# Kernel optimization log

Measured on AMD Instinct MI355X. Metric: run time of the kernel, lower is better.

## Reference

```python
import jax, jax.numpy as jnp
import numpy as np
import math

NUM_HEADS = 16
D_MODEL = 1024
LN_EPS = 1e-5


def _layer_norm(x, g, b):
    mu = jnp.mean(x, axis=-1, keepdims=True)
    var = jnp.mean((x - mu) ** 2, axis=-1, keepdims=True)
    return (x - mu) / jnp.sqrt(var + LN_EPS) * g + b


def setup_inputs() -> dict:
    key = jax.random.key(0)
    ks = jax.random.split(key, 12)
    B, H, W, d = 32, 16, 16, D_MODEL
    P, F = 64, 128
    s = 0.02
    return {
        "x": jax.random.normal(ks[0], (B, H, W, d), jnp.float32),
        "pattern_features": jax.random.normal(ks[1], (B, P, F), jnp.float32),
        "wq": jax.random.normal(ks[2], (d, d), jnp.float32) * s,
        "bq": jnp.zeros((d,), jnp.float32),
        "wk": jax.random.normal(ks[3], (d, d), jnp.float32) * s,
        "bk": jnp.zeros((d,), jnp.float32),
        "wv": jax.random.normal(ks[4], (d, d), jnp.float32) * s,
        "bv": jnp.zeros((d,), jnp.float32),
        "wo": jax.random.normal(ks[5], (d, d), jnp.float32) * s,
        "bo": jnp.zeros((d,), jnp.float32),
        "ln_g": jnp.ones((d,), jnp.float32),
        "ln_b": jnp.zeros((d,), jnp.float32),
    }


def reference(x, pattern_features, wq, bq, wk, bk, wv, bv, wo, bo, ln_g, ln_b):
    B, H, W, d = x.shape
    S = H * W
    nh = NUM_HEADS
    dk = d // nh
    x_seq = x.reshape(B, S, d)

    def proj(w, b):
        return (x_seq @ w.T + b).reshape(B, S, nh, dk).transpose(0, 2, 1, 3)  # (B,nh,S,dk)

    q, k, v = proj(wq, bq), proj(wk, bk), proj(wv, bv)
    scores = jnp.einsum("bhsd,bhtd->bhst", q, k) / math.sqrt(dk)  # (B,nh,S,S)

    # creative bias: diversity bonus on top-left min(S,64) block, same for all heads
    m = min(S, 64)
    sim = jnp.einsum("bpf,bqf->bpq", pattern_features, pattern_features)
    div = 1.0 - jax.nn.softmax(sim, axis=-1)  # (B,P,P)
    bias = jnp.zeros((B, nh, S, S), x.dtype)
    bias = bias.at[:, :, :m, :m].set(div[:, None, :m, :m] * 0.1)

    # faithful to torch: scores + bias.unsqueeze(0) -> rank-5 (1,B,nh,S,S)
    scores5 = scores[None] + bias[None]
    aw = jax.nn.softmax(scores5, axis=-1)
    attn = jnp.matmul(aw, v)  # (1,B,nh,S,dk) via broadcasting
    # faithful to torch transpose(1,2).view(B,S,d): row-major reshape of (1,nh,B,S,dk)
    attn = jnp.transpose(attn, (0, 2, 1, 3, 4)).reshape(B, S, d)

    out = attn @ wo.T + bo
    out = _layer_norm(out + x_seq, ln_g, ln_b)

    attention_weights = jax.nn.softmax(scores, axis=-1).mean(axis=1)  # (B,S,S)
    return out.reshape(B, H, W, d), attention_weights
```

## Files before the change

kernel.cpp:

```cpp
#include <hip/hip_runtime.h>

typedef unsigned short u16;
typedef unsigned int   u32;
typedef short bf16x8 __attribute__((ext_vector_type(8)));
typedef float f32x4  __attribute__((ext_vector_type(4)));

__device__ __forceinline__ float bf2f(u16 u){
  union { u32 u; float f; } c; c.u = ((u32)u) << 16; return c.f;
}
__device__ __forceinline__ u16 f2bf(float f){
  union { float f; u32 u; } c; c.f = f;
  u32 u = c.u + 0x7fffu + ((c.u >> 16) & 1u);
  return (u16)(u >> 16);
}

__device__ __forceinline__ void gload16(const u16* g, u16* l){
  __builtin_amdgcn_global_load_lds((const __attribute__((address_space(1))) u32*)g,
                                   (__attribute__((address_space(3))) u32*)l, 16, 0, 0);
}

__device__ __forceinline__ float waveRed(float v, int ismax){
  #pragma unroll
  for (int o = 32; o > 0; o >>= 1){
    float t = __shfl_xor(v, o, 64);
    v = ismax ? fmaxf(v, t) : (v + t);
  }
  return v;
}
__device__ __forceinline__ float blockRed(float v, int ismax, float* red, int tid){
  v = waveRed(v, ismax);
  __syncthreads();
  if ((tid & 63) == 0) red[tid >> 6] = v;
  __syncthreads();
  return ismax ? fmaxf(fmaxf(red[0], red[1]), fmaxf(red[2], red[3]))
               : (red[0] + red[1] + red[2] + red[3]);
}

__global__ __launch_bounds__(256)
void conv_x(const float* __restrict__ src, u16* __restrict__ dst){
  const size_t i = ((size_t)blockIdx.x * 256 + threadIdx.x) * 8;
  const float4 a = *(const float4*)(src + i);
  const float4 b = *(const float4*)(src + i + 4);
  uint4 o;
  o.x = (u32)f2bf(a.x) | ((u32)f2bf(a.y) << 16);
  o.y = (u32)f2bf(a.z) | ((u32)f2bf(a.w) << 16);
  o.z = (u32)f2bf(b.x) | ((u32)f2bf(b.y) << 16);
  o.w = (u32)f2bf(b.z) | ((u32)f2bf(b.w) << 16);
  *(uint4*)(dst + i) = o;
}

__global__ __launch_bounds__(256)
void conv_w4(const float* __restrict__ w0, const float* __restrict__ w1,
             const float* __restrict__ w2, const float* __restrict__ w3,
             u16* __restrict__ dst){
  const float* s = blockIdx.y == 0 ? w0 : (blockIdx.y == 1 ? w1 : (blockIdx.y == 2 ? w2 : w3));
  u16* d = dst + (size_t)blockIdx.y * 1048576;
  const size_t i = ((size_t)blockIdx.x * 256 + threadIdx.x) * 8;
  const float4 a = *(const float4*)(s + i);
  const float4 b = *(const float4*)(s + i + 4);
  uint4 o;
  o.x = (u32)f2bf(a.x) | ((u32)f2bf(a.y) << 16);
  o.y = (u32)f2bf(a.z) | ((u32)f2bf(a.w) << 16);
  o.z = (u32)f2bf(b.x) | ((u32)f2bf(b.y) << 16);
  o.w = (u32)f2bf(b.z) | ((u32)f2bf(b.w) << 16);
  *(uint4*)(d + i) = o;
}

__global__ __launch_bounds__(256)
void div_kernel(const float* __restrict__ pf, float* __restrict__ divp)
{
  __shared__ float pfs[64][129];
  __shared__ float svs[64][65];
  const int b = blockIdx.x;
  const int tid = threadIdx.x;
  const float* pb = pf + (size_t)b * 8192;
  for (int i = tid; i < 8192; i += 256) pfs[i >> 7][i & 127] = pb[i];
  __syncthreads();
  const int p = tid & 63, qg = tid >> 6;
  for (int qq = qg * 16; qq < qg * 16 + 16; ++qq){
    float a = 0.f;
    #pragma unroll 8
    for (int f = 0; f < 128; ++f) a += pfs[p][f] * pfs[qq][f];
    svs[p][qq] = a;
  }
  __syncthreads();
  if (tid < 64){
    float m = -1e30f;
    for (int qq = 0; qq < 64; ++qq) m = fmaxf(m, svs[tid][qq]);
    float s = 0.f;
    for (int qq = 0; qq < 64; ++qq){ const float e = __expf(svs[tid][qq] - m); svs[tid][qq] = e; s += e; }
    const float inv = 1.f / s;
    float* dr = divp + ((size_t)b * 64 + tid) * 64;
    for (int qq = 0; qq < 64; ++qq) dr[qq] = 0.1f * (1.f - svs[tid][qq] * inv);
  }
}

template<int MODE>
__global__ __launch_bounds__(256, 3)
void gemm_lds(const u16* __restrict__ A, const u16* __restrict__ Wb,
              const float* __restrict__ bias0, const float* __restrict__ bias1,
              const float* __restrict__ bias2, void* __restrict__ outp)
{
  __shared__ u16 As[3][4096];
  __shared__ u16 Bs[3][4096];
  const int tid = threadIdx.x, lane = tid & 63, w = tid >> 6;
  const int wm = (w >> 1) * 64, wn = (w & 1) * 64;
  const int bm = blockIdx.x;
  int bn = blockIdx.y;
  const u16* Wp = Wb;
  const float* bias = bias0;
  float scale = 1.f;
  int wsel = 0;
  if (MODE == 0){
    wsel = bn >> 3; bn &= 7;
    Wp = Wb + (size_t)wsel * 1048576;
    bias = wsel == 0 ? bias0 : (wsel == 1 ? bias1 : bias2);
    if (wsel == 0) scale = 0.125f;
  }

  const f32x4 z = {0.f, 0.f, 0.f, 0.f};
  f32x4 acc[4][4];
  #pragma unroll
  for (int i = 0; i < 4; ++i)
    #pragma unroll
    for (int j = 0; j < 4; ++j) acc[i][j] = z;

  const int r4  = lane >> 2;
  const int c8s = (((lane & 3) ^ ((lane >> 3) & 3)) * 8);
  const int ca0 = w * 2, ca1 = w * 2 + 1;
  const u16* gA0 = A  + (size_t)(bm * 128 + ca0 * 16 + r4) * 1024 + c8s;
  const u16* gA1 = A  + (size_t)(bm * 128 + ca1 * 16 + r4) * 1024 + c8s;
  const u16* gB0 = Wp + (size_t)(bn * 128 + ca0 * 16 + r4) * 1024 + c8s;
  const u16* gB1 = Wp + (size_t)(bn * 128 + ca1 * 16 + r4) * 1024 + c8s;
  const int lo0 = ca0 * 512 + lane * 8;
  const int lo1 = ca1 * 512 + lane * 8;

  const int fr = lane & 15, quad = lane >> 4;
  int offA[4], offB[4];
  #pragma unroll
  for (int i = 0; i < 4; ++i){
    const int r = wm + i * 16 + fr;
    offA[i] = r * 32 + ((quad ^ ((r >> 1) & 3)) * 8);
  }
  #pragma unroll
  for (int j = 0; j < 4; ++j){
    const int r = wn + j * 16 + fr;
    offB[j] = r * 32 + ((quad ^ ((r >> 1) & 3)) * 8);
  }

#define STG(s, kk) \
    gload16(gA0 + (kk), &As[s][lo0]); \
    gload16(gA1 + (kk), &As[s][lo1]); \
    gload16(gB0 + (kk), &Bs[s][lo0]); \
    gload16(gB1 + (kk), &Bs[s][lo1]);

  STG(0, 0)
  STG(1, 32)
  asm volatile("s_waitcnt vmcnt(4)" ::: "memory");
  __builtin_amdgcn_sched_barrier(0);
  __builtin_amdgcn_s_barrier();
  asm volatile("" ::: "memory");
  __builtin_amdgcn_sched_barrier(0);

  int slot = 0;
  #pragma unroll 1
  for (int t = 0; t < 32; ++t){
    const int s2 = slot < 1 ? 2 : slot - 1;
    if (t < 30){ STG(s2, (t + 2) * 32) }
    const u16* as_ = As[slot];
    const u16* bs_ = Bs[slot];
    bf16x8 af[4], bfv[4];
    #pragma unroll
    for (int i = 0; i < 4; ++i) af[i]  = *(const bf16x8*)&as_[offA[i]];
    #pragma unroll
    for (int j = 0; j < 4; ++j) bfv[j] = *(const bf16x8*)&bs_[offB[j]];
    __builtin_amdgcn_s_setprio(1);
    #pragma unroll
    for (int i = 0; i < 4; ++i)
      #pragma unroll
      for (int j = 0; j < 4; ++j)
        acc[i][j] = __builtin_amdgcn_mfma_f32_16x16x32_bf16(af[i], bfv[j], acc[i][j], 0, 0, 0);
    __builtin_amdgcn_s_setprio(0);
    if (t < 30)       { asm volatile("s_waitcnt vmcnt(4)" ::: "memory"); }
    else if (t == 30) { asm volatile("s_waitcnt vmcnt(0)" ::: "memory"); }
    if (t < 31){
      __builtin_amdgcn_sched_barrier(0);
      __builtin_amdgcn_s_barrier();
      asm volatile("" ::: "memory");
      __builtin_amdgcn_sched_barrier(0);
    }
    slot = slot == 2 ? 0 : slot + 1;
  }
#undef STG

  #pragma unroll
  for (int i = 0; i < 4; ++i){
    #pragma unroll
    for (int j = 0; j < 4; ++j){
      const int gr0 = bm * 128 + wm + i * 16 + ((lane >> 4) * 4);
      const int gc  = bn * 128 + wn + j * 16 + (lane & 15);
      const float bvv = bias[gc];
      #pragma unroll
      for (int r = 0; r < 4; ++r){
        const int gr = gr0 + r;
        const float val = (acc[i][j][r] + bvv) * scale;
        if (MODE == 0){
          const int b = gr >> 8, s = gr & 255, h = gc >> 6, kk = gc & 63;
          ((u16*)outp)[(size_t)wsel * 8388608 + (size_t)b * 262144 +
                       (size_t)h * 16384 + (size_t)s * 64 + kk] = f2bf(val);
        } else {
          ((float*)outp)[(size_t)gr * 1024 + gc] = val;
        }
      }
    }
  }
}

__global__ __launch_bounds__(256)
void attn_mfma(const u16* __restrict__ q, const u16* __restrict__ k,
               const u16* __restrict__ v, const float* __restrict__ divp,
               u16* __restrict__ attn_s)
{
  __shared__ u16 Vt[64][264];
  __shared__ u16 Ps[4][16][136];
  const int bh = blockIdx.x;
  const int b = bh >> 4, h = bh & 15;
  const int tid = threadIdx.x, lane = tid & 63, w = tid >> 6;
  const int quad = lane >> 4, l15 = lane & 15;
  const u16* kh = k + (size_t)bh * 16384;
  const u16* vh = v + (size_t)bh * 16384;
  const u16* qh = q + (size_t)bh * 16384;

  #pragma unroll
  for (int c = 0; c < 4; ++c){
    const int pidx = tid + c * 256;
    const int t2 = pidx & 127;
    const int n0 = (pidx >> 7) * 8;
    const uint4 a  = *(const uint4*)(vh + (2 * t2) * 64 + n0);
    const uint4 bb = *(const uint4*)(vh + (2 * t2 + 1) * 64 + n0);
    const u32 aa[4] = {a.x, a.y, a.z, a.w};
    const u32 bb4[4] = {bb.x, bb.y, bb.z, bb.w};
    #pragma unroll
    for (int j2 = 0; j2 < 4; ++j2){
      const u32 lo = aa[j2], hi = bb4[j2];
      *(u32*)&Vt[n0 + 2 * j2    ][2 * t2] = (lo & 0xffffu) | (hi << 16);
      *(u32*)&Vt[n0 + 2 * j2 + 1][2 * t2] = (lo >> 16) | (hi & 0xffff0000u);
    }
  }
  __syncthreads();

  const f32x4 z = {0.f, 0.f, 0.f, 0.f};
  const int bp = 2 * h + (b >> 4);
  for (int i = 0; i < 4; ++i){
    const int row0 = w * 64 + i * 16;
    const bf16x8 af0 = *(const bf16x8*)(qh + (size_t)(row0 + l15) * 64 + quad * 8);
    const bf16x8 af1 = *(const bf16x8*)(qh + (size_t)(row0 + l15) * 64 + 32 + quad * 8);
    f32x4 sc[16];
    #pragma unroll
    for (int ct = 0; ct < 16; ++ct){
      const bf16x8 b0 = *(const bf16x8*)(kh + (size_t)(ct * 16 + l15) * 64 + quad * 8);
      const bf16x8 b1 = *(const bf16x8*)(kh + (size_t)(ct * 16 + l15) * 64 + 32 + quad * 8);
      f32x4 a = __builtin_amdgcn_mfma_f32_16x16x32_bf16(af0, b0, z, 0, 0, 0);
      sc[ct]  = __builtin_amdgcn_mfma_f32_16x16x32_bf16(af1, b1, a, 0, 0, 0);
    }
    if (w == 0){
      const float* dv = divp + (size_t)b * 4096 + (size_t)(i * 16 + quad * 4) * 64 + l15;
      #pragma unroll
      for (int ct = 0; ct < 4; ++ct)
        #pragma unroll
        for (int rr = 0; rr < 4; ++rr)
          sc[ct][rr] += dv[rr * 64 + ct * 16];
    }
    float rs[4];
    #pragma unroll
    for (int rr = 0; rr < 4; ++rr){
      float m = sc[0][rr];
      #pragma unroll
      for (int ct = 1; ct < 16; ++ct) m = fmaxf(m, sc[ct][rr]);
      #pragma unroll
      for (int o = 1; o < 16; o <<= 1) m = fmaxf(m, __shfl_xor(m, o, 64));
      float s = 0.f;
      #pragma unroll
      for (int ct = 0; ct < 16; ++ct){
        const float e = __expf(sc[ct][rr] - m); sc[ct][rr] = e; s += e;
      }
      #pragma unroll
      for (int o = 1; o < 16; o <<= 1) s += __shfl_xor(s, o, 64);
      rs[rr] = 1.f / s;
    }
    f32x4 o4[4] = {z, z, z, z};
    #pragma unroll
    for (int half = 0; half < 2; ++half){
      #pragma unroll
      for (int ct = 0; ct < 8; ++ct)
        #pragma unroll
        for (int rr = 0; rr < 4; ++rr)
          Ps[w][quad * 4 + rr][ct * 16 + l15] = f2bf(sc[half * 8 + ct][rr] * rs[rr]);
      #pragma unroll
      for (int kc = 0; kc < 4; ++kc){
        const bf16x8 pa = *(const bf16x8*)&Ps[w][l15][kc * 32 + quad * 8];
        #pragma unroll
        for (int nt = 0; nt < 4; ++nt){
          const bf16x8 vb8 = *(const bf16x8*)&Vt[nt * 16 + l15][half * 128 + kc * 32 + quad * 8];
          o4[nt] = __builtin_amdgcn_mfma_f32_16x16x32_bf16(pa, vb8, o4[nt], 0, 0, 0);
        }
      }
    }
    const int sp = (b & 15) * 16 + (w * 4 + i);
    #pragma unroll
    for (int nt = 0; nt < 4; ++nt)
      #pragma unroll
      for (int rr = 0; rr < 4; ++rr){
        const int slo = quad * 4 + rr;
        const int cp = slo * 64 + nt * 16 + l15;
        attn_s[((size_t)bp * 256 + sp) * 1024 + cp] = f2bf(o4[nt][rr]);
      }
  }
}

__global__ __launch_bounds__(256)
void aw_kernel(const u16* __restrict__ q, const u16* __restrict__ k,
               float* __restrict__ aw)
{
  __shared__ float redm[16][4];
  __shared__ float reds[16][4];
  const int blk = blockIdx.x;
  const int b = blk >> 4, st = blk & 15;
  const int tid = threadIdx.x, lane = tid & 63, w = tid >> 6;
  const int quad = lane >> 4, l15 = lane & 15;
  const int rowb = st * 16;
  const f32x4 z = {0.f, 0.f, 0.f, 0.f};
  float awacc[4][4] = {};
  for (int h = 0; h < 16; ++h){
    const u16* kh = k + (((size_t)b * 16 + h) * 16384);
    const u16* qh = q + (((size_t)b * 16 + h) * 16384);
    const bf16x8 af0 = *(const bf16x8*)(qh + (size_t)(rowb + l15) * 64 + quad * 8);
    const bf16x8 af1 = *(const bf16x8*)(qh + (size_t)(rowb + l15) * 64 + 32 + quad * 8);
    f32x4 sc[4];
    #pragma unroll
    for (int j4 = 0; j4 < 4; ++j4){
      const int ct = w * 4 + j4;
      const bf16x8 b0 = *(const bf16x8*)(kh + (size_t)(ct * 16 + l15) * 64 + quad * 8);
      const bf16x8 b1 = *(const bf16x8*)(kh + (size_t)(ct * 16 + l15) * 64 + 32 + quad * 8);
      f32x4 a = __builtin_amdgcn_mfma_f32_16x16x32_bf16(af0, b0, z, 0, 0, 0);
      sc[j4]  = __builtin_amdgcn_mfma_f32_16x16x32_bf16(af1, b1, a, 0, 0, 0);
    }
    float pm[4];
    #pragma unroll
    for (int rr = 0; rr < 4; ++rr){
      float m = fmaxf(fmaxf(sc[0][rr], sc[1][rr]), fmaxf(sc[2][rr], sc[3][rr]));
      #pragma unroll
      for (int o = 1; o < 16; o <<= 1) m = fmaxf(m, __shfl_xor(m, o, 64));
      pm[rr] = m;
    }
    if (l15 == 0)
      #pragma unroll
      for (int rr = 0; rr < 4; ++rr) redm[quad * 4 + rr][w] = pm[rr];
    __syncthreads();
    float ps[4];
    #pragma unroll
    for (int rr = 0; rr < 4; ++rr){
      const int row = quad * 4 + rr;
      const float m = fmaxf(fmaxf(redm[row][0], redm[row][1]),
                            fmaxf(redm[row][2], redm[row][3]));
      float s = 0.f;
      #pragma unroll
      for (int j4 = 0; j4 < 4; ++j4){
        const float e = __expf(sc[j4][rr] - m); sc[j4][rr] = e; s += e;
      }
      #pragma unroll
      for (int o = 1; o < 16; o <<= 1) s += __shfl_xor(s, o, 64);
      ps[rr] = s;
    }
    if (l15 == 0)
      #pragma unroll
      for (int rr = 0; rr < 4; ++rr) reds[quad * 4 + rr][w] = ps[rr];
    __syncthreads();
    #pragma unroll
    for (int rr = 0; rr < 4; ++rr){
      const int row = quad * 4 + rr;
      const float inv = 1.f / (reds[row][0] + reds[row][1] + reds[row][2] + reds[row][3]);
      #pragma unroll
      for (int j4 = 0; j4 < 4; ++j4) awacc[j4][rr] += sc[j4][rr] * inv;
    }
  }
  const size_t base = (size_t)b * 65536;
  #pragma unroll
  for (int j4 = 0; j4 < 4; ++j4){
    const int col = (w * 4 + j4) * 16 + l15;
    #pragma unroll
    for (int rr = 0; rr < 4; ++rr){
      const int row = rowb + quad * 4 + rr;
      aw[base + (size_t)row * 256 + col] = awacc[j4][rr] * 0.0625f;
    }
  }
}

__global__ __launch_bounds__(256)
void ln_kernel(const float* __restrict__ y2, const float* __restrict__ x,
               const float* __restrict__ g, const float* __restrict__ bb,
               float* __restrict__ outp)
{
  __shared__ float red[4];
  const int r = blockIdx.x, tid = threadIdx.x;
  const float4 yv = ((const float4*)(y2 + (size_t)r * 1024))[tid];
  const float4 xv = ((const float4*)(x  + (size_t)r * 1024))[tid];
  const float v0 = yv.x + xv.x;
  const float v1 = yv.y + xv.y;
  const float v2 = yv.z + xv.z;
  const float v3 = yv.w + xv.w;
  const float ssum = blockRed(v0 + v1 + v2 + v3, 0, red, tid);
  const float mu = ssum * (1.f / 1024.f);
  const float d0 = v0 - mu, d1 = v1 - mu, d2 = v2 - mu, d3 = v3 - mu;
  const float sq = blockRed(d0 * d0 + d1 * d1 + d2 * d2 + d3 * d3, 0, red, tid);
  const float rstd = rsqrtf(sq * (1.f / 1024.f) + 1e-5f);
  const float4 gv = ((const float4*)g)[tid];
  const float4 bv = ((const float4*)bb)[tid];
  float4 o;
  o.x = d0 * rstd * gv.x + bv.x;
  o.y = d1 * rstd * gv.y + bv.y;
  o.z = d2 * rstd * gv.z + bv.z;
  o.w = d3 * rstd * gv.w + bv.w;
  ((float4*)(outp + (size_t)r * 1024))[tid] = o;
}

extern "C" void kernel_launch(void* const* d_in, const int* in_sizes, int n_in,
                              void* d_out, int out_size, void* d_ws, size_t ws_size,
                              hipStream_t stream)
{
  int ix = -1, ipf = -1, iw[4] = {-1,-1,-1,-1}, iv[6] = {-1,-1,-1,-1,-1,-1};
  int nw = 0, nv = 0;
  for (int i = 0; i < n_in; ++i){
    const int sz = in_sizes[i];
    if (sz == 8388608 && ix < 0) ix = i;
    else if (sz == 262144 && ipf < 0) ipf = i;
    else if (sz == 1048576 && nw < 4) iw[nw++] = i;
    else if (sz == 1024 && nv < 6) iv[nv++] = i;
  }
  if (ix < 0 || ipf < 0 || nw != 4 || nv != 6){
    ix = 0; ipf = 1; iw[0] = 2; iv[0] = 3; iw[1] = 4; iv[1] = 5;
    iw[2] = 6; iv[2] = 7; iw[3] = 8; iv[3] = 9; iv[4] = 10; iv[5] = 11;
  }

  const float* x   = (const float*)d_in[ix];
  const float* pf  = (const float*)d_in[ipf];
  const float* wq  = (const float*)d_in[iw[0]];
  const float* wk  = (const float*)d_in[iw[1]];
  const float* wv  = (const float*)d_in[iw[2]];
  const float* wo  = (const float*)d_in[iw[3]];
  const float* bq  = (const float*)d_in[iv[0]];
  const float* bk  = (const float*)d_in[iv[1]];
  const float* bv  = (const float*)d_in[iv[2]];
  const float* bo  = (const float*)d_in[iv[3]];
  const float* lng = (const float*)d_in[iv[4]];
  const float* lnb = (const float*)d_in[iv[5]];

  float* out0   = (float*)d_out;
  float* aw_out = out0 + 8388608;

  u16* x_bf = (u16*)d_out;
  u16* attn = x_bf + 8388608;
  u16* qkv    = (u16*)d_ws;
  float* divp = (float*)((char*)d_ws + (size_t)48 * 1048576);
  u16* warena = (u16*)((char*)d_ws + (size_t)49 * 1048576);
  float* y2   = (float*)d_ws;

  conv_x<<<4096, 256, 0, stream>>>(x, x_bf);
  conv_w4<<<dim3(512, 4), 256, 0, stream>>>(wq, wk, wv, wo, warena);
  div_kernel<<<32, 256, 0, stream>>>(pf, divp);

  gemm_lds<0><<<dim3(64, 24), 256, 0, stream>>>(x_bf, warena, bq, bk, bv, (void*)qkv);

  u16* qw = qkv, *kw = qkv + 8388608, *vw = qkv + 16777216;
  attn_mfma<<<512, 256, 0, stream>>>(qw, kw, vw, divp, attn);
  aw_kernel<<<512, 256, 0, stream>>>(qw, kw, aw_out);

  gemm_lds<1><<<dim3(64, 8), 256, 0, stream>>>(attn, warena + 3145728, bo, nullptr, nullptr, (void*)y2);
  ln_kernel<<<8192, 256, 0, stream>>>(y2, x, lng, lnb, out0);
}
```

Before: 330.2 us.

## Use 256x256-tile 512-thread QKV GEMM and merge conversion kernels

Replaces the QKV projection GEMM with a new kernel using 256x256 output tiles, 8 waves per block and a triple-buffered LDS pipeline, raising per-block data reuse and cutting grid size. It also fuses the x and weight fp32-to-bf16 conversion launches into one kernel to save a launch. The larger tile uses much more LDS and registers (128 accumulator floats per lane), which lowers occupancy and risks spills. The scattered per-element bf16 output stores remain.

Measured after the change: 353.8 us. +7.1%, slower.

```diff
diff --git a/kernel.cpp b/kernel.cpp
--- a/kernel.cpp
+++ b/kernel.cpp
@@ -37,25 +37,24 @@
 }
 
 __global__ __launch_bounds__(256)
-void conv_x(const float* __restrict__ src, u16* __restrict__ dst){
-  const size_t i = ((size_t)blockIdx.x * 256 + threadIdx.x) * 8;
-  const float4 a = *(const float4*)(src + i);
-  const float4 b = *(const float4*)(src + i + 4);
-  uint4 o;
-  o.x = (u32)f2bf(a.x) | ((u32)f2bf(a.y) << 16);
-  o.y = (u32)f2bf(a.z) | ((u32)f2bf(a.w) << 16);
-  o.z = (u32)f2bf(b.x) | ((u32)f2bf(b.y) << 16);
-  o.w = (u32)f2bf(b.z) | ((u32)f2bf(b.w) << 16);
-  *(uint4*)(dst + i) = o;
-}
-
-__global__ __launch_bounds__(256)
-void conv_w4(const float* __restrict__ w0, const float* __restrict__ w1,
-             const float* __restrict__ w2, const float* __restrict__ w3,
-             u16* __restrict__ dst){
-  const float* s = blockIdx.y == 0 ? w0 : (blockIdx.y == 1 ? w1 : (blockIdx.y == 2 ? w2 : w3));
-  u16* d = dst + (size_t)blockIdx.y * 1048576;
-  const size_t i = ((size_t)blockIdx.x * 256 + threadIdx.x) * 8;
+void conv_all(const float* __restrict__ x, const float* __restrict__ w0,
+              const float* __restrict__ w1, const float* __restrict__ w2,
+              const float* __restrict__ w3, u16* __restrict__ xdst,
+              u16* __restrict__ wdst){
+  const int bid = blockIdx.x;
+  const float* s;
+  u16* d;
+  size_t i;
+  if (bid < 4096){
+    s = x; d = xdst;
+    i = ((size_t)bid * 256 + threadIdx.x) * 8;
+  } else {
+    const int wb = bid - 4096;
+    const int wi = wb >> 9;
+    s = wi == 0 ? w0 : (wi == 1 ? w1 : (wi == 2 ? w2 : w3));
+    d = wdst + (size_t)wi * 1048576;
+    i = ((size_t)(wb & 511) * 256 + threadIdx.x) * 8;
+  }
   const float4 a = *(const float4*)(s + i);
   const float4 b = *(const float4*)(s + i + 4);
   uint4 o;
@@ -92,6 +91,116 @@
     const float inv = 1.f / s;
     float* dr = divp + ((size_t)b * 64 + tid) * 64;
     for (int qq = 0; qq < 64; ++qq) dr[qq] = 0.1f * (1.f - svs[tid][qq] * inv);
+  }
+}
+
+__global__ __launch_bounds__(512, 2)
+void gemm_qkv(const u16* __restrict__ A, const u16* __restrict__ Wb,
+              const float* __restrict__ bias0, const float* __restrict__ bias1,
+              const float* __restrict__ bias2, u16* __restrict__ outp)
+{
+  __shared__ u16 As[3][8192];
+  __shared__ u16 Bs[3][8192];
+  const int tid = threadIdx.x, lane = tid & 63, w = tid >> 6;
+  const int wm = (w >> 2) * 128, wn = (w & 3) * 64;
+  const int bm = blockIdx.x;
+  const int y  = blockIdx.y;
+  const int wsel = y >> 2, bn = y & 3;
+  const u16* Wp = Wb + (size_t)wsel * 1048576;
+  const float* bias = wsel == 0 ? bias0 : (wsel == 1 ? bias1 : bias2);
+  const float scale = wsel == 0 ? 0.125f : 1.f;
+
+  const f32x4 z = {0.f, 0.f, 0.f, 0.f};
+  f32x4 acc[8][4];
+  #pragma unroll
+  for (int i = 0; i < 8; ++i)
+    #pragma unroll
+    for (int j = 0; j < 4; ++j) acc[i][j] = z;
+
+  const int r4  = lane >> 2;
+  const int c8s = (((lane & 3) ^ ((lane >> 3) & 3)) * 8);
+  const int ca0 = w * 2, ca1 = w * 2 + 1;
+  const u16* gA0 = A  + (size_t)(bm * 256 + ca0 * 16 + r4) * 1024 + c8s;
+  const u16* gA1 = A  + (size_t)(bm * 256 + ca1 * 16 + r4) * 1024 + c8s;
+  const u16* gB0 = Wp + (size_t)(bn * 256 + ca0 * 16 + r4) * 1024 + c8s;
+  const u16* gB1 = Wp + (size_t)(bn * 256 + ca1 * 16 + r4) * 1024 + c8s;
+  const int lo0 = ca0 * 512 + lane * 8;
+  const int lo1 = ca1 * 512 + lane * 8;
+
+  const int fr = lane & 15, quad = lane >> 4;
+  int offA[8], offB[4];
+  #pragma unroll
+  for (int i = 0; i < 8; ++i){
+    const int r = wm + i * 16 + fr;
+    offA[i] = r * 32 + ((quad ^ ((r >> 1) & 3)) * 8);
+  }
+  #pragma unroll
+  for (int j = 0; j < 4; ++j){
+    const int r = wn + j * 16 + fr;
+    offB[j] = r * 32 + ((quad ^ ((r >> 1) & 3)) * 8);
+  }
+
+#define STG(s, kk) \
+    gload16(gA0 + (kk), &As[s][lo0]); \
+    gload16(gA1 + (kk), &As[s][lo1]); \
+    gload16(gB0 + (kk), &Bs[s][lo0]); \
+    gload16(gB1 + (kk), &Bs[s][lo1]);
+
+  STG(0, 0)
+  STG(1, 32)
+  asm volatile("s_waitcnt vmcnt(4)" ::: "memory");
+  __builtin_amdgcn_sched_barrier(0);
+  __builtin_amdgcn_s_barrier();
+  asm volatile("" ::: "memory");
+  __builtin_amdgcn_sched_barrier(0);
+
+  int slot = 0;
+  #pragma unroll 1
+  for (int t = 0; t < 32; ++t){
+    const int s2 = slot < 1 ? 2 : slot - 1;
+    if (t < 30){ STG(s2, (t + 2) * 32) }
+    const u16* as_ = As[slot];
+    const u16* bs_ = Bs[slot];
+    bf16x8 af[8], bfv[4];
+    #pragma unroll
+    for (int i = 0; i < 8; ++i) af[i]  = *(const bf16x8*)&as_[offA[i]];
+    #pragma unroll
+    for (int j = 0; j < 4; ++j) bfv[j] = *(const bf16x8*)&bs_[offB[j]];
+    __builtin_amdgcn_s_setprio(1);
+    #pragma unroll
+    for (int i = 0; i < 8; ++i)
+      #pragma unroll
+      for (int j = 0; j < 4; ++j)
+        acc[i][j] = __builtin_amdgcn_mfma_f32_16x16x32_bf16(af[i], bfv[j], acc[i][j], 0, 0, 0);
+    __builtin_amdgcn_s_setprio(0);
+    if (t < 30)       { asm volatile("s_waitcnt vmcnt(4)" ::: "memory"); }
+    else if (t == 30) { asm volatile("s_waitcnt vmcnt(0)" ::: "memory"); }
+    if (t < 31){
+      __builtin_amdgcn_sched_barrier(0);
+      __builtin_amdgcn_s_barrier();
+      asm volatile("" ::: "memory");
+      __builtin_amdgcn_sched_barrier(0);
+    }
+    slot = slot == 2 ? 0 : slot + 1;
+  }
+#undef STG
+
+  #pragma unroll
+  for (int i = 0; i < 8; ++i){
+    #pragma unroll
+    for (int j = 0; j < 4; ++j){
+      const int gr0 = bm * 256 + wm + i * 16 + quad * 4;
+      const int gc  = bn * 256 + wn + j * 16 + fr;
+      const float bvv = bias[gc];
+      #pragma unroll
+      for (int r = 0; r < 4; ++r){
+        const int gr = gr0 + r;
+        const float val = (acc[i][j][r] + bvv) * scale;
+        const int b = gr >> 8, s = gr & 255, h = gc >> 6, kk = gc & 63;
+        outp[(size_t)wsel * 8388608 + (size_t)b * 262144 +
+             (size_t)h * 16384 + (size_t)s * 64 + kk] = f2bf(val);
+      }
+    }
   }
 }
 
@@ -465,11 +574,10 @@
   u16* warena = (u16*)((char*)d_ws + (size_t)49 * 1048576);
   float* y2   = (float*)d_ws;
 
-  conv_x<<<4096, 256, 0, stream>>>(x, x_bf);
-  conv_w4<<<dim3(512, 4), 256, 0, stream>>>(wq, wk, wv, wo, warena);
+  conv_all<<<6144, 256, 0, stream>>>(x, wq, wk, wv, wo, x_bf, warena);
   div_kernel<<<32, 256, 0, stream>>>(pf, divp);
 
-  gemm_lds<0><<<dim3(64, 24), 256, 0, stream>>>(x_bf, warena, bq, bk, bv, (void*)qkv);
+  gemm_qkv<<<dim3(32, 12), 512, 0, stream>>>(x_bf, warena, bq, bk, bv, qkv);
 
   u16* qw = qkv, *kw = qkv + 8388608, *vw = qkv + 16777216;
   attn_mfma<<<512, 256, 0, stream>>>(qw, kw, vw, divp, attn);
```
